# Kernel optimization log

Hardware: AMD Instinct MI355X
Metric: run time of the kernel (lower is better)

## Reference

```python
import jax, jax.numpy as jnp
import numpy as np

NUM_HEADS = 16
EPS = 1e-6
ROPE_THETA = 10000.0


def _rmsnorm_fp32(x, w):
    # RMSNorm computed in fp32, scale by learned weight (per head_dim)
    xf = x.astype(jnp.float32)
    var = jnp.mean(xf * xf, axis=-1, keepdims=True)
    return (xf * jax.lax.rsqrt(var + EPS) * w.astype(jnp.float32)).astype(x.dtype)


def _rope_3d_angles(T, H, W, head_dim):
    # split head_dim across (t,h,w) axes; all parts even
    dh = 2 * ((head_dim // 3) // 2)
    dw = dh
    dt = head_dim - dh - dw

    def axis_ang(L, d):
        inv = 1.0 / (ROPE_THETA ** (jnp.arange(0, d, 2, dtype=jnp.float32) / d))
        return jnp.arange(L, dtype=jnp.float32)[:, None] * inv[None, :]  # [L, d//2]

    at = axis_ang(T, dt)  # [T, dt/2]
    ah = axis_ang(H, dh)  # [H, dh/2]
    aw = axis_ang(W, dw)  # [W, dw/2]
    # broadcast to [T,H,W, head_dim//2] then flatten to [N, head_dim//2]
    at_g = jnp.broadcast_to(at[:, None, None, :], (T, H, W, dt // 2))
    ah_g = jnp.broadcast_to(ah[None, :, None, :], (T, H, W, dh // 2))
    aw_g = jnp.broadcast_to(aw[None, None, :, :], (T, H, W, dw // 2))
    ang = jnp.concatenate([at_g, ah_g, aw_g], axis=-1).reshape(T * H * W, head_dim // 2)
    return jnp.cos(ang), jnp.sin(ang)


def _apply_rope(x, cos, sin):
    # x: [B,Hh,N,D]; cos/sin: [N, D/2]; interleaved complex-pair rotation
    xr = x[..., 0::2]
    xi = x[..., 1::2]
    c = cos[None, None, :, :]
    s = sin[None, None, :, :]
    out_r = xr * c - xi * s
    out_i = xr * s + xi * c
    return jnp.stack([out_r, out_i], axis=-1).reshape(x.shape)


def setup_inputs() -> dict:
    key = jax.random.key(0)
    ks = jax.random.split(key, 7)
    dim, hd = 2048, 128
    x = jax.random.normal(ks[0], (1, 2048, dim), dtype=jnp.float32)
    qkv_w = jax.random.normal(ks[1], (3 * dim, dim), dtype=jnp.float32) * (dim ** -0.5)
    qkv_b = jax.random.normal(ks[2], (3 * dim,), dtype=jnp.float32) * 0.02
    proj_w = jax.random.normal(ks[3], (dim, dim), dtype=jnp.float32) * (dim ** -0.5)
    proj_b = jax.random.normal(ks[4], (dim,), dtype=jnp.float32) * 0.02
    q_norm_w = jnp.ones((hd,), dtype=jnp.float32)
    k_norm_w = jnp.ones((hd,), dtype=jnp.float32)
    return {"x": x, "qkv_w": qkv_w, "qkv_b": qkv_b, "proj_w": proj_w,
            "proj_b": proj_b, "q_norm_w": q_norm_w, "k_norm_w": k_norm_w,
            "t_dim": 8, "h_dim": 16, "w_dim": 16}


def reference(x, qkv_w, qkv_b, proj_w, proj_b, q_norm_w, k_norm_w, t_dim, h_dim, w_dim):
    B, N, C = x.shape
    Hh = NUM_HEADS
    D = C // Hh
    scale = D ** -0.5
    # QKV projection (torch Linear: x @ W.T + b)
    qkv = x @ qkv_w.T + qkv_b                      # [B,N,3C]
    qkv = qkv.reshape(B, N, 3, Hh, D).transpose(2, 0, 3, 1, 4)  # [3,B,Hh,N,D]
    q, k, v = qkv[0], qkv[1], qkv[2]
    q = _rmsnorm_fp32(q, q_norm_w)
    k = _rmsnorm_fp32(k, k_norm_w)
    cos, sin = _rope_3d_angles(t_dim, h_dim, w_dim, D)
    q = _apply_rope(q, cos, sin)
    k = _apply_rope(k, cos, sin)
    # SDPA (non-causal)
    scores = jnp.einsum('bhqd,bhkd->bhqk', q, k) * scale
    attn = jax.nn.softmax(scores, axis=-1)
    out = jnp.einsum('bhqk,bhkd->bhqd', attn, v)   # [B,Hh,N,D]
    out = out.transpose(0, 2, 1, 3).reshape(B, N, C)
    return out @ proj_w.T + proj_b
```

## Files before the change

### kernel.cpp

```cpp
#include <hip/hip_runtime.h>
#include <hip/hip_bf16.h>
#include <cstdint>
#include <cstddef>

typedef __attribute__((ext_vector_type(8))) short bf16x8;
typedef __attribute__((ext_vector_type(4))) float f32x4;

#define AS1 __attribute__((address_space(1)))
#define AS3 __attribute__((address_space(3)))

__device__ __forceinline__ void gload_lds16(const void* g, void* l) {
  __builtin_amdgcn_global_load_lds((const AS1 void*)g, (AS3 void*)l, 16, 0, 0);
}

__device__ __forceinline__ unsigned short f2bf(float x) {
  __hip_bfloat16 h = __float2bfloat16(x);
  return __builtin_bit_cast(unsigned short, h);
}

__global__ __launch_bounds__(256) void k_cvt_bf16(const float* __restrict__ in,
                                                  unsigned short* __restrict__ out,
                                                  int n4) {
  int i = blockIdx.x * 256 + threadIdx.x;
  const int stride = gridDim.x * 256;
  for (; i < n4; i += stride) {
    float4 v = reinterpret_cast<const float4*>(in)[i];
    ushort4 o;
    o.x = f2bf(v.x); o.y = f2bf(v.y); o.z = f2bf(v.z); o.w = f2bf(v.w);
    reinterpret_cast<ushort4*>(out)[i] = o;
  }
}

__global__ __launch_bounds__(256) void k_rope_tab(float* __restrict__ cosT,
                                                  float* __restrict__ sinT,
                                                  const int* __restrict__ hdim,
                                                  const int* __restrict__ wdim) {
  int idx = blockIdx.x * 256 + threadIdx.x;
  if (idx >= 2048 * 64) return;
  const int n = idx >> 6, j = idx & 63;
  const int H = *hdim, W = *wdim;
  const int w = n % W;
  const int rem = n / W;
  const int h = rem % H;
  const int t = rem / H;
  float pos, i2, d;
  if (j < 22)      { pos = (float)t; i2 = (float)(2 * j);        d = 44.f; }
  else if (j < 43) { pos = (float)h; i2 = (float)(2 * (j - 22)); d = 42.f; }
  else             { pos = (float)w; i2 = (float)(2 * (j - 43)); d = 42.f; }
  const float ang = pos * powf(10000.0f, -i2 / d);
  cosT[idx] = cosf(ang);
  sinT[idx] = sinf(ang);
}

__global__ __launch_bounds__(512, 2) void k_gemm256(const unsigned short* __restrict__ A,
                                                    const unsigned short* __restrict__ B,
                                                    const float* __restrict__ bias,
                                                    float* __restrict__ C,
                                                    int M, int N, int K) {
  __shared__ __align__(16) char lds[131072];
  const int tid = threadIdx.x;
  const int lane = tid & 63;
  const int wid = tid >> 6;
  const int wr = wid >> 2, wc = wid & 3;

  const int nbx = N >> 8;
  const int cpx = gridDim.x >> 3;
  const int swz = (blockIdx.x & 7) * cpx + (blockIdx.x >> 3);
  const int by = swz / nbx, bx = swz % nbx;
  const int row0 = by * 256, col0 = bx * 256;
  const int NT = K >> 6;

  auto stage_slot = [&](const unsigned short* src, int grow0, int kcol0, char* slot) {
#pragma unroll
    for (int r = 0; r < 2; ++r) {
      const int off = r * 8192 + tid * 16;
      const int pair = off >> 7;
      const int un = (off & 127) ^ ((pair & 7) << 4);
      const int grow = pair * 2 + (un >> 6);
      gload_lds16(src + (size_t)(grow0 + grow) * K + kcol0 + ((un & 63) >> 1),
                  slot + r * 8192 + wid * 1024);
    }
  };
  auto frag = [&](const char* slot, int r, int kb) -> bf16x8 {
    return *reinterpret_cast<const bf16x8*>(
        slot + (r >> 1) * 128 + ((((r & 1) << 6) + kb) ^ (((r >> 1) & 7) << 4)));
  };

  f32x4 acc[8][4];
#pragma unroll
  for (int i = 0; i < 8; ++i)
#pragma unroll
    for (int j = 0; j < 4; ++j) acc[i][j] = (f32x4){0.f, 0.f, 0.f, 0.f};

  stage_slot(A, row0, 0,  lds);
  stage_slot(B, col0, 0,  lds + 65536);
  stage_slot(A, row0, 32, lds + 16384);
  stage_slot(B, col0, 32, lds + 65536 + 16384);
  asm volatile("s_waitcnt vmcnt(4)" ::: "memory");
  __builtin_amdgcn_s_barrier();

  const int kb = (lane >> 4) << 4;
  for (int j = 0; j < NT; ++j) {
    const int b = j & 1, bp = b ^ 1;
    const char* A0 = lds + (2 * b + 0) * 16384;
    const char* A1 = lds + (2 * b + 1) * 16384;
    const char* B0 = lds + 65536 + (2 * b + 0) * 16384;
    const char* B1 = lds + 65536 + (2 * b + 1) * 16384;
    char* pA0 = lds + (2 * bp + 0) * 16384;
    char* pA1 = lds + (2 * bp + 1) * 16384;
    char* pB0 = lds + 65536 + (2 * bp + 0) * 16384;
    char* pB1 = lds + 65536 + (2 * bp + 1) * 16384;
    const bool pf = (j + 1 < NT);
    const int kn = (j + 1) * 64;
    bf16x8 af[8], bq[2];

#pragma unroll
    for (int rf = 0; rf < 8; ++rf) af[rf] = frag(A0, wr * 128 + rf * 16 + (lane & 15), kb);
#pragma unroll
    for (int cf = 0; cf < 2; ++cf) bq[cf] = frag(B0, wc * 64 + cf * 16 + (lane & 15), kb);
    if (pf) stage_slot(A, row0, kn, pA0);
    __builtin_amdgcn_s_barrier();
    __builtin_amdgcn_s_setprio(1);
#pragma unroll
    for (int rf = 0; rf < 8; ++rf)
#pragma unroll
      for (int cf = 0; cf < 2; ++cf)
        acc[rf][cf] = __builtin_amdgcn_mfma_f32_16x16x32_bf16(af[rf], bq[cf], acc[rf][cf], 0, 0, 0);
    __builtin_amdgcn_s_setprio(0);
    __builtin_amdgcn_s_barrier();

#pragma unroll
    for (int cf = 0; cf < 2; ++cf) bq[cf] = frag(B0, wc * 64 + (cf + 2) * 16 + (lane & 15), kb);
    if (pf) stage_slot(B, col0, kn, pB0);
    if (pf) asm volatile("s_waitcnt vmcnt(4)" ::: "memory");
    else    asm volatile("s_waitcnt vmcnt(0)" ::: "memory");
    __builtin_amdgcn_s_barrier();
    __builtin_amdgcn_s_setprio(1);
#pragma unroll
    for (int rf = 0; rf < 8; ++rf)
#pragma unroll
      for (int cf = 0; cf < 2; ++cf)
        acc[rf][cf + 2] = __builtin_amdgcn_mfma_f32_16x16x32_bf16(af[rf], bq[cf], acc[rf][cf + 2], 0, 0, 0);
    __builtin_amdgcn_s_setprio(0);
    __builtin_amdgcn_s_barrier();

#pragma unroll
    for (int rf = 0; rf < 8; ++rf) af[rf] = frag(A1, wr * 128 + rf * 16 + (lane & 15), kb);
#pragma unroll
    for (int cf = 0; cf < 2; ++cf) bq[cf] = frag(B1, wc * 64 + cf * 16 + (lane & 15), kb);
    if (pf) stage_slot(A, row0, kn + 32, pA1);
    __builtin_amdgcn_s_barrier();
    __builtin_amdgcn_s_setprio(1);
#pragma unroll
    for (int rf = 0; rf < 8; ++rf)
#pragma unroll
      for (int cf = 0; cf < 2; ++cf)
        acc[rf][cf] = __builtin_amdgcn_mfma_f32_16x16x32_bf16(af[rf], bq[cf], acc[rf][cf], 0, 0, 0);
    __builtin_amdgcn_s_setprio(0);
    __builtin_amdgcn_s_barrier();

#pragma unroll
    for (int cf = 0; cf < 2; ++cf) bq[cf] = frag(B1, wc * 64 + (cf + 2) * 16 + (lane & 15), kb);
    if (pf) stage_slot(B, col0, kn + 32, pB1);
    if (pf) asm volatile("s_waitcnt vmcnt(4)" ::: "memory");
    __builtin_amdgcn_s_barrier();
    __builtin_amdgcn_s_setprio(1);
#pragma unroll
    for (int rf = 0; rf < 8; ++rf)
#pragma unroll
      for (int cf = 0; cf < 2; ++cf)
        acc[rf][cf + 2] = __builtin_amdgcn_mfma_f32_16x16x32_bf16(af[rf], bq[cf], acc[rf][cf + 2], 0, 0, 0);
    __builtin_amdgcn_s_setprio(0);
    __builtin_amdgcn_s_barrier();
  }

#pragma unroll
  for (int fr = 0; fr < 8; ++fr)
#pragma unroll
    for (int fc = 0; fc < 4; ++fc) {
      const int col = col0 + wc * 64 + fc * 16 + (lane & 15);
      const float bv = bias[col];
#pragma unroll
      for (int jj = 0; jj < 4; ++jj) {
        const int row = row0 + wr * 128 + fr * 16 + (lane >> 4) * 4 + jj;
        C[(size_t)row * N + col] = acc[fr][fc][jj] + bv;
      }
    }
}

__global__ __launch_bounds__(256) void k_gemm_bt(const unsigned short* __restrict__ A,
                                                 const unsigned short* __restrict__ B,
                                                 const float* __restrict__ bias,
                                                 float* __restrict__ C,
                                                 int M, int N, int K) {
  __shared__ __align__(16) unsigned short As[128 * 32];
  __shared__ __align__(16) unsigned short Bs[128 * 32];
  const int lane = threadIdx.x & 63;
  const int wid  = threadIdx.x >> 6;
  const int wr = wid >> 1, wc = wid & 1;
  const int rowA0 = blockIdx.y * 128;
  const int rowB0 = blockIdx.x * 128;

  f32x4 acc[4][4];
#pragma unroll
  for (int i = 0; i < 4; ++i)
#pragma unroll
    for (int j = 0; j < 4; ++j) acc[i][j] = (f32x4){0.f, 0.f, 0.f, 0.f};

  for (int kt = 0; kt < K; kt += 32) {
#pragma unroll
    for (int i = 0; i < 2; ++i) {
      const int c = i * 4 + wid;
      const int off = c * 1024 + lane * 16;
      const int row = off >> 6;
      const int col = (off & 63) >> 1;
      gload_lds16(A + (size_t)(rowA0 + row) * K + kt + col, (char*)As + c * 1024);
      gload_lds16(B + (size_t)(rowB0 + row) * K + kt + col, (char*)Bs + c * 1024);
    }
    __syncthreads();
    bf16x8 af[4], bfr[4];
#pragma unroll
    for (int mi = 0; mi < 4; ++mi)
      af[mi] = *reinterpret_cast<const bf16x8*>(
          &As[(wr * 64 + mi * 16 + (lane & 15)) * 32 + (lane >> 4) * 8]);
#pragma unroll
    for (int ni = 0; ni < 4; ++ni)
      bfr[ni] = *reinterpret_cast<const bf16x8*>(
          &Bs[(wc * 64 + ni * 16 + (lane & 15)) * 32 + (lane >> 4) * 8]);
#pragma unroll
    for (int mi = 0; mi < 4; ++mi)
#pragma unroll
      for (int ni = 0; ni < 4; ++ni)
        acc[mi][ni] = __builtin_amdgcn_mfma_f32_16x16x32_bf16(af[mi], bfr[ni], acc[mi][ni], 0, 0, 0);
    __syncthreads();
  }

#pragma unroll
  for (int mi = 0; mi < 4; ++mi)
#pragma unroll
    for (int ni = 0; ni < 4; ++ni) {
      const int col = rowB0 + wc * 64 + ni * 16 + (lane & 15);
      const float b = bias[col];
#pragma unroll
      for (int j = 0; j < 4; ++j) {
        const int row = rowA0 + wr * 64 + mi * 16 + (lane >> 4) * 4 + j;
        C[(size_t)row * N + col] = acc[mi][ni][j] + b;
      }
    }
}

__global__ __launch_bounds__(256) void k_qk_post(const float* __restrict__ qkv,
                                                 const float* __restrict__ qw,
                                                 const float* __restrict__ kw,
                                                 const float* __restrict__ cosT,
                                                 const float* __restrict__ sinT,
                                                 unsigned short* __restrict__ qo,
                                                 unsigned short* __restrict__ ko) {
  const int lane = threadIdx.x & 63;
  const int wid = threadIdx.x >> 6;
  const int pair = blockIdx.x * 4 + wid;
  const int n = pair >> 4, h = pair & 15;
  const float c = cosT[n * 64 + lane];
  const float s = sinT[n * 64 + lane];
#pragma unroll
  for (int sq = 0; sq < 2; ++sq) {
    const float* src = qkv + (size_t)n * 6144 + sq * 2048 + h * 128;
    float2 v = reinterpret_cast<const float2*>(src)[lane];
    float ss = v.x * v.x + v.y * v.y;
#pragma unroll
    for (int m = 1; m < 64; m <<= 1) ss += __shfl_xor(ss, m, 64);
    const float r = rsqrtf(ss * (1.0f / 128.0f) + 1e-6f);
    float2 wv = reinterpret_cast<const float2*>(sq == 0 ? qw : kw)[lane];
    const float xr = v.x * r * wv.x;
    const float xi = v.y * r * wv.y;
    float orr = xr * c - xi * s;
    float oi  = xr * s + xi * c;
    if (sq == 0) { orr *= 0.08838834764831845f; oi *= 0.08838834764831845f; }
    unsigned short* dst = (sq == 0 ? qo : ko) + ((size_t)h * 2048 + n) * 128 + 2 * lane;
    const unsigned int pk = (unsigned int)f2bf(orr) | ((unsigned int)f2bf(oi) << 16);
    *reinterpret_cast<unsigned int*>(dst) = pk;
  }
}

__global__ __launch_bounds__(256) void k_v_tr(const float* __restrict__ qkv,
                                              unsigned short* __restrict__ vt) {
  __shared__ __align__(16) unsigned short tile[64][130];
  const int h = blockIdx.y;
  const int n0 = blockIdx.x * 64;
  const int t = threadIdx.x;
  {
    const int row = t >> 2;
    const int c0 = (t & 3) * 32;
    const float* src = qkv + (size_t)(n0 + row) * 6144 + 4096 + h * 128 + c0;
#pragma unroll
    for (int j = 0; j < 32; j += 4) {
      float4 v = reinterpret_cast<const float4*>(src + j)[0];
      tile[row][c0 + j + 0] = f2bf(v.x);
      tile[row][c0 + j + 1] = f2bf(v.y);
      tile[row][c0 + j + 2] = f2bf(v.z);
      tile[row][c0 + j + 3] = f2bf(v.w);
    }
  }
  __syncthreads();
  {
    const int d = t >> 1;
    const int nc = (t & 1) * 32;
    unsigned short* dst = vt + ((size_t)h * 128 + d) * 2048 + n0 + nc;
#pragma unroll
    for (int j = 0; j < 32; j += 8) {
      bf16x8 o;
#pragma unroll
      for (int jj = 0; jj < 8; ++jj) o[jj] = (short)tile[nc + j + jj][d];
      *reinterpret_cast<bf16x8*>(dst + j) = o;
    }
  }
}

__global__ __launch_bounds__(256) void k_fattn(const unsigned short* __restrict__ q,
                                               const unsigned short* __restrict__ k,
                                               const unsigned short* __restrict__ vt,
                                               unsigned short* __restrict__ out) {
  __shared__ __align__(16) unsigned short Ks[2][64 * 128];
  __shared__ __align__(16) unsigned short Vs[2][128 * 64];
  __shared__ __align__(16) unsigned short Ps[4][16][72];
  const int lane = threadIdx.x & 63;
  const int wid = threadIdx.x >> 6;
  const int h = blockIdx.x & 15;
  const int qb = blockIdx.x >> 4;
  const int q0 = qb * 64 + wid * 16;

  auto stage = [&](int buf, int kt) {
#pragma unroll
    for (int i = 0; i < 4; ++i) {
      const int c = i * 4 + wid;
      const int off = c * 1024 + lane * 16;
      const int krow = off >> 8;
      const int kcb = (off & 255) ^ ((krow & 7) << 4);
      gload_lds16(k + ((size_t)h * 2048 + kt * 64 + krow) * 128 + (kcb >> 1),
                  (char*)Ks[buf] + c * 1024);
      const int vrow = off >> 7;
      const int vcb = (off & 127) ^ ((vrow & 7) << 4);
      gload_lds16(vt + ((size_t)h * 128 + vrow) * 2048 + kt * 64 + (vcb >> 1),
                  (char*)Vs[buf] + c * 1024);
    }
  };

  bf16x8 qf[4];
  {
    const unsigned short* qp = q + ((size_t)h * 2048 + q0 + (lane & 15)) * 128 + (lane >> 4) * 8;
#pragma unroll
    for (int kc = 0; kc < 4; ++kc) qf[kc] = *reinterpret_cast<const bf16x8*>(qp + kc * 32);
  }
  f32x4 O[8];
#pragma unroll
  for (int i = 0; i < 8; ++i) O[i] = (f32x4){0.f, 0.f, 0.f, 0.f};
  float m = -1e30f, l = 0.f;

  stage(0, 0);
  __syncthreads();

  for (int kt = 0; kt < 32; ++kt) {
    const int cur = kt & 1;
    if (kt < 31) stage(cur ^ 1, kt + 1);

    f32x4 sf[4];
    __builtin_amdgcn_s_setprio(1);
#pragma unroll
    for (int ni = 0; ni < 4; ++ni) {
      f32x4 a = (f32x4){0.f, 0.f, 0.f, 0.f};
      const int key = ni * 16 + (lane & 15);
#pragma unroll
      for (int kc = 0; kc < 4; ++kc) {
        const int db = (kc * 64 + (lane >> 4) * 16) ^ ((key & 7) << 4);
        bf16x8 af = *reinterpret_cast<const bf16x8*>((const char*)Ks[cur] + key * 256 + db);
        a = __builtin_amdgcn_mfma_f32_16x16x32_bf16(af, qf[kc], a, 0, 0, 0);
      }
      sf[ni] = a;
    }
    __builtin_amdgcn_s_setprio(0);

    float mt = fmaxf(fmaxf(sf[0][0], sf[0][1]), fmaxf(sf[0][2], sf[0][3]));
#pragma unroll
    for (int ni = 1; ni < 4; ++ni)
      mt = fmaxf(mt, fmaxf(fmaxf(sf[ni][0], sf[ni][1]), fmaxf(sf[ni][2], sf[ni][3])));
    mt = fmaxf(mt, __shfl_xor(mt, 16, 64));
    mt = fmaxf(mt, __shfl_xor(mt, 32, 64));

    if (!__all(mt <= m + 8.0f)) {
      const float mn = fmaxf(m, mt);
      const float al = __expf(m - mn);
      m = mn;
      l *= al;
#pragma unroll
      for (int dc = 0; dc < 8; ++dc)
#pragma unroll
        for (int j = 0; j < 4; ++j) O[dc][j] *= al;
    }
    float rs = 0.f;
#pragma unroll
    for (int ni = 0; ni < 4; ++ni)
#pragma unroll
      for (int j = 0; j < 4; ++j) {
        const float p = __expf(sf[ni][j] - m);
        sf[ni][j] = p;
        rs += p;
      }
    rs += __shfl_xor(rs, 16, 64);
    rs += __shfl_xor(rs, 32, 64);
    l += rs;

#pragma unroll
    for (int ni = 0; ni < 4; ++ni) {
      ushort4 pk;
      pk.x = f2bf(sf[ni][0]); pk.y = f2bf(sf[ni][1]);
      pk.z = f2bf(sf[ni][2]); pk.w = f2bf(sf[ni][3]);
      *reinterpret_cast<ushort4*>(&Ps[wid][lane & 15][ni * 16 + (lane >> 4) * 4]) = pk;
    }
    bf16x8 pa[2];
#pragma unroll
    for (int ks = 0; ks < 2; ++ks)
      pa[ks] = *reinterpret_cast<const bf16x8*>(&Ps[wid][lane & 15][ks * 32 + (lane >> 4) * 8]);

    __builtin_amdgcn_s_setprio(1);
#pragma unroll
    for (int dc = 0; dc < 8; ++dc) {
      const int d = dc * 16 + (lane & 15);
#pragma unroll
      for (int ks = 0; ks < 2; ++ks) {
        const int kb2 = (ks * 64 + (lane >> 4) * 16) ^ ((d & 7) << 4);
        bf16x8 af = *reinterpret_cast<const bf16x8*>((const char*)Vs[cur] + d * 128 + kb2);
        O[dc] = __builtin_amdgcn_mfma_f32_16x16x32_bf16(af, pa[ks], O[dc], 0, 0, 0);
      }
    }
    __builtin_amdgcn_s_setprio(0);
    __syncthreads();
  }

  const float rl = 1.0f / l;
  const int qrow = q0 + (lane & 15);
#pragma unroll
  for (int dc = 0; dc < 8; ++dc) {
    ushort4 o;
    o.x = f2bf(O[dc][0] * rl); o.y = f2bf(O[dc][1] * rl);
    o.z = f2bf(O[dc][2] * rl); o.w = f2bf(O[dc][3] * rl);
    *reinterpret_cast<ushort4*>(
        &out[(size_t)qrow * 2048 + h * 128 + dc * 16 + (lane >> 4) * 4]) = o;
  }
}

extern "C" void kernel_launch(void* const* d_in, const int* in_sizes, int n_in,
                              void* d_out, int out_size, void* d_ws, size_t ws_size,
                              hipStream_t stream) {
  (void)in_sizes; (void)n_in; (void)out_size; (void)ws_size;
  const float* x      = (const float*)d_in[0];
  const float* qkv_w  = (const float*)d_in[1];
  const float* qkv_b  = (const float*)d_in[2];
  const float* proj_w = (const float*)d_in[3];
  const float* proj_b = (const float*)d_in[4];
  const float* q_nw   = (const float*)d_in[5];
  const float* k_nw   = (const float*)d_in[6];
  const int* h_dim    = (const int*)d_in[8];
  const int* w_dim    = (const int*)d_in[9];
  float* out = (float*)d_out;

  char* ws = (char*)d_ws;
  size_t off = 0;
  auto carve = [&](size_t bytes) -> void* {
    void* p = ws + off;
    off += (bytes + 255) & ~(size_t)255;
    return p;
  };
  unsigned short* x_bf   = (unsigned short*)carve(2048ull * 2048 * 2);
  unsigned short* w1_bf  = (unsigned short*)carve(6144ull * 2048 * 2);
  unsigned short* w2_bf  = (unsigned short*)carve(2048ull * 2048 * 2);
  float*          qkvf   = (float*)carve(2048ull * 6144 * 4);
  unsigned short* q_bf   = (unsigned short*)carve(16ull * 2048 * 128 * 2);
  unsigned short* k_bf   = (unsigned short*)carve(16ull * 2048 * 128 * 2);
  unsigned short* vt_bf  = (unsigned short*)carve(16ull * 2048 * 128 * 2);
  unsigned short* att_bf = (unsigned short*)carve(2048ull * 2048 * 2);
  float*          cosT   = (float*)carve(2048ull * 64 * 4);
  float*          sinT   = (float*)carve(2048ull * 64 * 4);

  hipLaunchKernelGGL(k_cvt_bf16, dim3(2048), dim3(256), 0, stream, x, x_bf, 2048 * 2048 / 4);
  hipLaunchKernelGGL(k_cvt_bf16, dim3(2048), dim3(256), 0, stream, qkv_w, w1_bf, 6144 * 2048 / 4);
  hipLaunchKernelGGL(k_cvt_bf16, dim3(2048), dim3(256), 0, stream, proj_w, w2_bf, 2048 * 2048 / 4);
  hipLaunchKernelGGL(k_rope_tab, dim3(512), dim3(256), 0, stream, cosT, sinT, h_dim, w_dim);
  hipLaunchKernelGGL(k_gemm256, dim3(192), dim3(512), 0, stream,
                     x_bf, w1_bf, qkv_b, qkvf, 2048, 6144, 2048);
  hipLaunchKernelGGL(k_qk_post, dim3(8192), dim3(256), 0, stream,
                     qkvf, q_nw, k_nw, cosT, sinT, q_bf, k_bf);
  hipLaunchKernelGGL(k_v_tr, dim3(32, 16), dim3(256), 0, stream, qkvf, vt_bf);
  hipLaunchKernelGGL(k_fattn, dim3(512), dim3(256), 0, stream, q_bf, k_bf, vt_bf, att_bf);
  hipLaunchKernelGGL(k_gemm_bt, dim3(16, 16), dim3(256), 0, stream,
                     att_bf, w2_bf, proj_b, out, 2048, 2048, 2048);
}
```

Before: 207.6 us.

## Switch attention to 32x32 MFMA with split-K and fragment-ordered V

The flash attention kernel now uses 32x32x16 MFMA tiles with 32 query rows per wave and 128 queries per block. The key range is split in two across blocks, and a new merge kernel combines the halves using per-row log-sum-exp. V is pre-transposed into a fragment-ready layout so each lane loads its MFMA operand straight from global memory, and V is no longer staged in LDS. This cuts LDS traffic and instruction count per FLOP and keeps 512 blocks, at the cost of an extra merge pass, an extra bf16 partial-output buffer, and uncached global V loads inside the inner loop.

```diff
diff --git a/kernel.cpp b/kernel.cpp
--- a/kernel.cpp
+++ b/kernel.cpp
@@ -5,6 +5,7 @@
 
 typedef __attribute__((ext_vector_type(8))) short bf16x8;
 typedef __attribute__((ext_vector_type(4))) float f32x4;
+typedef __attribute__((ext_vector_type(16))) float f32x16;
 
 #define AS1 __attribute__((address_space(1)))
 #define AS3 __attribute__((address_space(3)))
@@ -16,6 +17,9 @@
 __device__ __forceinline__ unsigned short f2bf(float x) {
   __hip_bfloat16 h = __float2bfloat16(x);
   return __builtin_bit_cast(unsigned short, h);
+}
+__device__ __forceinline__ float bf2f(unsigned short u) {
+  return __builtin_bit_cast(float, (unsigned int)u << 16);
 }
 
 __global__ __launch_bounds__(256) void k_cvt_bf16(const float* __restrict__ in,
@@ -283,7 +287,7 @@
 }
 
 __global__ __launch_bounds__(256) void k_v_tr(const float* __restrict__ qkv,
-                                              unsigned short* __restrict__ vt) {
+                                              unsigned short* __restrict__ vt2) {
   __shared__ __align__(16) unsigned short tile[64][130];
   const int h = blockIdx.y;
   const int n0 = blockIdx.x * 64;
@@ -302,88 +306,95 @@
     }
   }
   __syncthreads();
-  {
-    const int d = t >> 1;
-    const int nc = (t & 1) * 32;
-    unsigned short* dst = vt + ((size_t)h * 128 + d) * 2048 + n0 + nc;
-#pragma unroll
-    for (int j = 0; j < 32; j += 8) {
-      bf16x8 o;
-#pragma unroll
-      for (int jj = 0; jj < 8; ++jj) o[jj] = (short)tile[nc + j + jj][d];
-      *reinterpret_cast<bf16x8*>(dst + j) = o;
-    }
+#pragma unroll
+  for (int g4 = 0; g4 < 4; ++g4) {
+    const int g = g4 * 256 + t;
+    const int c = g >> 8;
+    const int dblk = (g >> 6) & 3;
+    const int p = g & 63;
+    const int d = dblk * 32 + (p & 31);
+    const int hi = p >> 5;
+    bf16x8 o;
+#pragma unroll
+    for (int e = 0; e < 8; ++e) o[e] = (short)tile[c * 16 + hi * 8 + e][d];
+    const size_t oidx = ((((size_t)h * 128 + (n0 >> 4) + c) * 4 + dblk) * 64 + p) * 8;
+    *reinterpret_cast<bf16x8*>(vt2 + oidx) = o;
   }
 }
 
 __global__ __launch_bounds__(256) void k_fattn(const unsigned short* __restrict__ q,
                                                const unsigned short* __restrict__ k,
-                                               const unsigned short* __restrict__ vt,
-                                               unsigned short* __restrict__ out) {
+                                               const unsigned short* __restrict__ vt2,
+                                               unsigned short* __restrict__ Onorm,
+                                               float* __restrict__ lseb) {
   __shared__ __align__(16) unsigned short Ks[2][64 * 128];
-  __shared__ __align__(16) unsigned short Vs[2][128 * 64];
-  __shared__ __align__(16) unsigned short Ps[4][16][72];
+  __shared__ __align__(16) unsigned short Ps[4][32][72];
   const int lane = threadIdx.x & 63;
   const int wid = threadIdx.x >> 6;
-  const int h = blockIdx.x & 15;
-  const int qb = blockIdx.x >> 4;
-  const int q0 = qb * 64 + wid * 16;
-
-  auto stage = [&](int buf, int kt) {
-#pragma unroll
-    for (int i = 0; i < 4; ++i) {
-      const int c = i * 4 + wid;
-      const int off = c * 1024 + lane * 16;
-      const int krow = off >> 8;
-      const int kcb = (off & 255) ^ ((krow & 7) << 4);
-      gload_lds16(k + ((size_t)h * 2048 + kt * 64 + krow) * 128 + (kcb >> 1),
-                  (char*)Ks[buf] + c * 1024);
-      const int vrow = off >> 7;
-      const int vcb = (off & 127) ^ ((vrow & 7) << 4);
-      gload_lds16(vt + ((size_t)h * 128 + vrow) * 2048 + kt * 64 + (vcb >> 1),
-                  (char*)Vs[buf] + c * 1024);
+  const int hi2 = lane >> 5;
+  const int ql = lane & 31;
+  const int bid = blockIdx.x;
+  const int h = bid & 15;
+  const int qb = (bid >> 4) & 15;
+  const int ksp = bid >> 8;
+  const int q0 = qb * 128 + wid * 32;
+  const int kbase = ksp * 1024;
+
+  auto stageK = [&](int buf, int kt2) {
+#pragma unroll
+    for (int r = 0; r < 4; ++r) {
+      const int off = r * 4096 + (wid * 64 + lane) * 16;
+      const int row = off >> 8;
+      const int colb = (off & 255) ^ ((row & 15) << 4);
+      gload_lds16(k + ((size_t)h * 2048 + kbase + kt2 * 64 + row) * 128 + (colb >> 1),
+                  (char*)Ks[buf] + r * 4096 + wid * 1024);
     }
   };
 
-  bf16x8 qf[4];
+  bf16x8 qf[8];
   {
-    const unsigned short* qp = q + ((size_t)h * 2048 + q0 + (lane & 15)) * 128 + (lane >> 4) * 8;
-#pragma unroll
-    for (int kc = 0; kc < 4; ++kc) qf[kc] = *reinterpret_cast<const bf16x8*>(qp + kc * 32);
-  }
-  f32x4 O[8];
-#pragma unroll
-  for (int i = 0; i < 8; ++i) O[i] = (f32x4){0.f, 0.f, 0.f, 0.f};
+    const unsigned short* qp = q + ((size_t)h * 2048 + q0 + ql) * 128 + hi2 * 8;
+#pragma unroll
+    for (int c = 0; c < 8; ++c) qf[c] = *reinterpret_cast<const bf16x8*>(qp + c * 16);
+  }
+  f32x16 O[4];
+#pragma unroll
+  for (int i = 0; i < 4; ++i)
+#pragma unroll
+    for (int j = 0; j < 16; ++j) O[i][j] = 0.f;
   float m = -1e30f, l = 0.f;
 
-  stage(0, 0);
+  stageK(0, 0);
   __syncthreads();
 
-  for (int kt = 0; kt < 32; ++kt) {
+  const int kswz = (lane & 15) << 4;
+  for (int kt = 0; kt < 16; ++kt) {
     const int cur = kt & 1;
-    if (kt < 31) stage(cur ^ 1, kt + 1);
-
-    f32x4 sf[4];
+    if (kt < 15) stageK(cur ^ 1, kt + 1);
+
+    f32x16 s0, s1;
+#pragma unroll
+    for (int j = 0; j < 16; ++j) { s0[j] = 0.f; s1[j] = 0.f; }
     __builtin_amdgcn_s_setprio(1);
 #pragma unroll
-    for (int ni = 0; ni < 4; ++ni) {
-      f32x4 a = (f32x4){0.f, 0.f, 0.f, 0.f};
-      const int key = ni * 16 + (lane & 15);
-#pragma unroll
-      for (int kc = 0; kc < 4; ++kc) {
-        const int db = (kc * 64 + (lane >> 4) * 16) ^ ((key & 7) << 4);
-        bf16x8 af = *reinterpret_cast<const bf16x8*>((const char*)Ks[cur] + key * 256 + db);
-        a = __builtin_amdgcn_mfma_f32_16x16x32_bf16(af, qf[kc], a, 0, 0, 0);
-      }
-      sf[ni] = a;
+    for (int c = 0; c < 8; ++c) {
+      bf16x8 a0 = *reinterpret_cast<const bf16x8*>(
+          (const char*)Ks[cur] + ql * 256 + ((c * 32 + hi2 * 16) ^ kswz));
+      s0 = __builtin_amdgcn_mfma_f32_32x32x16_bf16(a0, qf[c], s0, 0, 0, 0);
+    }
+#pragma unroll
+    for (int c = 0; c < 8; ++c) {
+      bf16x8 a1 = *reinterpret_cast<const bf16x8*>(
+          (const char*)Ks[cur] + (32 + ql) * 256 + ((c * 32 + hi2 * 16) ^ kswz));
+      s1 = __builtin_amdgcn_mfma_f32_32x32x16_bf16(a1, qf[c], s1, 0, 0, 0);
     }
     __builtin_amdgcn_s_setprio(0);
 
-    float mt = fmaxf(fmaxf(sf[0][0], sf[0][1]), fmaxf(sf[0][2], sf[0][3]));
-#pragma unroll
-    for (int ni = 1; ni < 4; ++ni)
-      mt = fmaxf(mt, fmaxf(fmaxf(sf[ni][0], sf[ni][1]), fmaxf(sf[ni][2], sf[ni][3])));
-    mt = fmaxf(mt, __shfl_xor(mt, 16, 64));
+    float mt = s0[0];
+#pragma unroll
+    for (int j = 1; j < 16; ++j) mt = fmaxf(mt, s0[j]);
+#pragma unroll
+    for (int j = 0; j < 16; ++j) mt = fmaxf(mt, s1[j]);
     mt = fmaxf(mt, __shfl_xor(mt, 32, 64));
 
     if (!__all(mt <= m + 8.0f)) {
@@ -392,44 +403,43 @@
       m = mn;
       l *= al;
 #pragma unroll
-      for (int dc = 0; dc < 8; ++dc)
-#pragma unroll
-        for (int j = 0; j < 4; ++j) O[dc][j] *= al;
+      for (int i = 0; i < 4; ++i)
+#pragma unroll
+        for (int j = 0; j < 16; ++j) O[i][j] *= al;
     }
     float rs = 0.f;
 #pragma unroll
-    for (int ni = 0; ni < 4; ++ni)
-#pragma unroll
-      for (int j = 0; j < 4; ++j) {
-        const float p = __expf(sf[ni][j] - m);
-        sf[ni][j] = p;
-        rs += p;
-      }
-    rs += __shfl_xor(rs, 16, 64);
+    for (int j = 0; j < 16; ++j) {
+      s0[j] = __expf(s0[j] - m); rs += s0[j];
+      s1[j] = __expf(s1[j] - m); rs += s1[j];
+    }
     rs += __shfl_xor(rs, 32, 64);
     l += rs;
 
 #pragma unroll
-    for (int ni = 0; ni < 4; ++ni) {
-      ushort4 pk;
-      pk.x = f2bf(sf[ni][0]); pk.y = f2bf(sf[ni][1]);
-      pk.z = f2bf(sf[ni][2]); pk.w = f2bf(sf[ni][3]);
-      *reinterpret_cast<ushort4*>(&Ps[wid][lane & 15][ni * 16 + (lane >> 4) * 4]) = pk;
-    }
-    bf16x8 pa[2];
-#pragma unroll
-    for (int ks = 0; ks < 2; ++ks)
-      pa[ks] = *reinterpret_cast<const bf16x8*>(&Ps[wid][lane & 15][ks * 32 + (lane >> 4) * 8]);
-
+    for (int a = 0; a < 4; ++a) {
+      uint2 w0, w1;
+      w0.x = (unsigned)f2bf(s0[a * 4 + 0]) | ((unsigned)f2bf(s0[a * 4 + 1]) << 16);
+      w0.y = (unsigned)f2bf(s0[a * 4 + 2]) | ((unsigned)f2bf(s0[a * 4 + 3]) << 16);
+      w1.x = (unsigned)f2bf(s1[a * 4 + 0]) | ((unsigned)f2bf(s1[a * 4 + 1]) << 16);
+      w1.y = (unsigned)f2bf(s1[a * 4 + 2]) | ((unsigned)f2bf(s1[a * 4 + 3]) << 16);
+      *reinterpret_cast<uint2*>(&Ps[wid][ql][a * 8 + hi2 * 4]) = w0;
+      *reinterpret_cast<uint2*>(&Ps[wid][ql][32 + a * 8 + hi2 * 4]) = w1;
+    }
+    bf16x8 pf[4];
+#pragma unroll
+    for (int c2 = 0; c2 < 4; ++c2)
+      pf[c2] = *reinterpret_cast<const bf16x8*>(&Ps[wid][ql][c2 * 16 + hi2 * 8]);
+
+    const int cg0 = (kbase >> 4) + kt * 4;
     __builtin_amdgcn_s_setprio(1);
 #pragma unroll
-    for (int dc = 0; dc < 8; ++dc) {
-      const int d = dc * 16 + (lane & 15);
-#pragma unroll
-      for (int ks = 0; ks < 2; ++ks) {
-        const int kb2 = (ks * 64 + (lane >> 4) * 16) ^ ((d & 7) << 4);
-        bf16x8 af = *reinterpret_cast<const bf16x8*>((const char*)Vs[cur] + d * 128 + kb2);
-        O[dc] = __builtin_amdgcn_mfma_f32_16x16x32_bf16(af, pa[ks], O[dc], 0, 0, 0);
+    for (int dblk = 0; dblk < 4; ++dblk) {
+#pragma unroll
+      for (int c2 = 0; c2 < 4; ++c2) {
+        bf16x8 va = *reinterpret_cast<const bf16x8*>(
+            vt2 + ((((size_t)h * 128 + cg0 + c2) * 4 + dblk) * 64 + lane) * 8);
+        O[dblk] = __builtin_amdgcn_mfma_f32_32x32x16_bf16(va, pf[c2], O[dblk], 0, 0, 0);
       }
     }
     __builtin_amdgcn_s_setprio(0);
@@ -437,15 +447,44 @@
   }
 
   const float rl = 1.0f / l;
-  const int qrow = q0 + (lane & 15);
-#pragma unroll
-  for (int dc = 0; dc < 8; ++dc) {
-    ushort4 o;
-    o.x = f2bf(O[dc][0] * rl); o.y = f2bf(O[dc][1] * rl);
-    o.z = f2bf(O[dc][2] * rl); o.w = f2bf(O[dc][3] * rl);
-    *reinterpret_cast<ushort4*>(
-        &out[(size_t)qrow * 2048 + h * 128 + dc * 16 + (lane >> 4) * 4]) = o;
-  }
+  const int n = q0 + ql;
+  unsigned short* ob = Onorm + (((size_t)(ksp * 16 + h) * 2048) + n) * 128;
+#pragma unroll
+  for (int dblk = 0; dblk < 4; ++dblk)
+#pragma unroll
+    for (int a = 0; a < 4; ++a) {
+      uint2 w;
+      w.x = (unsigned)f2bf(O[dblk][a * 4 + 0] * rl) | ((unsigned)f2bf(O[dblk][a * 4 + 1] * rl) << 16);
+      w.y = (unsigned)f2bf(O[dblk][a * 4 + 2] * rl) | ((unsigned)f2bf(O[dblk][a * 4 + 3] * rl) << 16);
+      *reinterpret_cast<uint2*>(ob + dblk * 32 + a * 8 + hi2 * 4) = w;
+    }
+  if (hi2 == 0)
+    lseb[(size_t)(ksp * 16 + h) * 2048 + n] = m + logf(l);
+}
+
+__global__ __launch_bounds__(256) void k_merge(const unsigned short* __restrict__ Onorm,
+                                               const float* __restrict__ lseb,
+                                               unsigned short* __restrict__ att) {
+  const int idx = blockIdx.x * 256 + threadIdx.x;
+  const int n = idx >> 8;
+  const int r = idx & 255;
+  const int h = r >> 4;
+  const int d0 = (r & 15) * 8;
+  const float l0 = lseb[(size_t)h * 2048 + n];
+  const float l1 = lseb[(size_t)(16 + h) * 2048 + n];
+  const float M = fmaxf(l0, l1);
+  float w0 = __expf(l0 - M), w1 = __expf(l1 - M);
+  const float inv = 1.0f / (w0 + w1);
+  w0 *= inv; w1 *= inv;
+  const bf16x8 o0 = *reinterpret_cast<const bf16x8*>(
+      Onorm + ((size_t)h * 2048 + n) * 128 + d0);
+  const bf16x8 o1 = *reinterpret_cast<const bf16x8*>(
+      Onorm + ((size_t)(16 + h) * 2048 + n) * 128 + d0);
+  bf16x8 o;
+#pragma unroll
+  for (int e = 0; e < 8; ++e)
+    o[e] = (short)f2bf(bf2f((unsigned short)o0[e]) * w0 + bf2f((unsigned short)o1[e]) * w1);
+  *reinterpret_cast<bf16x8*>(att + (size_t)n * 2048 + h * 128 + d0) = o;
 }
 
 extern "C" void kernel_launch(void* const* d_in, const int* in_sizes, int n_in,
@@ -476,8 +515,10 @@
   float*          qkvf   = (float*)carve(2048ull * 6144 * 4);
   unsigned short* q_bf   = (unsigned short*)carve(16ull * 2048 * 128 * 2);
   unsigned short* k_bf   = (unsigned short*)carve(16ull * 2048 * 128 * 2);
-  unsigned short* vt_bf  = (unsigned short*)carve(16ull * 2048 * 128 * 2);
+  unsigned short* vt2_bf = (unsigned short*)carve(16ull * 2048 * 128 * 2);
   unsigned short* att_bf = (unsigned short*)carve(2048ull * 2048 * 2);
+  unsigned short* on_bf  = (unsigned short*)carve(2ull * 16 * 2048 * 128 * 2);
+  float*          lseb   = (float*)carve(2ull * 16 * 2048 * 4);
   float*          cosT   = (float*)carve(2048ull * 64 * 4);
   float*          sinT   = (float*)carve(2048ull * 64 * 4);
 
@@ -489,8 +530,10 @@
                      x_bf, w1_bf, qkv_b, qkvf, 2048, 6144, 2048);
   hipLaunchKernelGGL(k_qk_post, dim3(8192), dim3(256), 0, stream,
                      qkvf, q_nw, k_nw, cosT, sinT, q_bf, k_bf);
-  hipLaunchKernelGGL(k_v_tr, dim3(32, 16), dim3(256), 0, stream, qkvf, vt_bf);
-  hipLaunchKernelGGL(k_fattn, dim3(512), dim3(256), 0, stream, q_bf, k_bf, vt_bf, att_bf);
+  hipLaunchKernelGGL(k_v_tr, dim3(32, 16), dim3(256), 0, stream, qkvf, vt2_bf);
+  hipLaunchKernelGGL(k_fattn, dim3(512), dim3(256), 0, stream,
+                     q_bf, k_bf, vt2_bf, on_bf, lseb);
+  hipLaunchKernelGGL(k_merge, dim3(2048), dim3(256), 0, stream, on_bf, lseb, att_bf);
   hipLaunchKernelGGL(k_gemm_bt, dim3(16, 16), dim3(256), 0, stream,
                      att_bf, w2_bf, proj_b, out, 2048, 2048, 2048);
 }
```

Result: slower. 219.1 us (+5.5%).
